# Kernel optimization log

Hardware: AMD Instinct MI355X
Metric: run time of the kernel (lower is better)

The kernel has to match this reference:

```python
import jax, jax.numpy as jnp
import numpy as np

B, S, D, H, K = 16, 2048, 1024, 16, 31  # batch, seq, d_model, n_heads, kernel_size


def setup_inputs() -> dict:
    key = jax.random.key(0)
    ks = jax.random.split(key, 6)
    sc = 1.0 / np.sqrt(D)
    return {
        "query_sequences": jax.random.normal(ks[0], (B, S, D), jnp.float32),
        "key_sequences": jax.random.normal(ks[1], (B, S, D), jnp.float32),
        "value_sequences": jax.random.normal(ks[2], (B, S, D), jnp.float32),
        "key_value_sequence_lengths": jax.random.randint(ks[3], (B,), 1, S + 1, jnp.int32),
        "W_q": jax.random.normal(ks[4], (D, H * K), jnp.float32) * sc,  # cast_queries.weight^T
        "b_q": jnp.zeros((H * K,), jnp.float32),                        # cast_queries.bias
        "conv_bias": jnp.zeros((H,), jnp.float32),
    }


def reference(query_sequences, key_sequences, value_sequences,
              key_value_sequence_lengths, W_q, b_q, conv_bias):
    b, s, d = query_sequences.shape
    h = conv_bias.shape[0]
    k = W_q.shape[1] // h
    r = d // h
    # Generate per-position, per-head depthwise filters from the queries.
    weights = (query_sequences @ W_q + b_q).reshape(b, s, h, k)  # (B,S,H,K)
    # Split key channels into heads and reduce within each head -> (B,S,H)
    ksum = key_sequences.reshape(b, s, h, r).sum(axis=-1)
    pad_l = (k - 1) // 2
    pad_r = k - 1 - pad_l
    kpad = jnp.pad(ksum, ((0, 0), (pad_l, pad_r), (0, 0)))  # (B, S+K-1, H)
    # Cross-correlation with per-position filters:
    # out[b,t,h] = sum_j weights[b,t,h,j] * kpad[b, t+j, h]
    out = jnp.zeros((b, s, h), dtype=weights.dtype)
    for j in range(k):  # fixed small kernel loop
        out = out + weights[..., j] * kpad[:, j:j + s, :]
    out = out + conv_bias  # per-head bias
    return out.transpose(0, 2, 1)  # (B, n_heads, S)
```

## Files before the change

### kernel.cpp

```cpp
#include <hip/hip_runtime.h>
#include <hip/hip_bf16.h>

#define BB 16
#define SS 2048
#define DD 1024
#define HH 16
#define KK 31
#define HK 496

typedef float f32x4 __attribute__((ext_vector_type(4)));
typedef __bf16 bf16x8 __attribute__((ext_vector_type(8)));

__device__ __forceinline__ unsigned short f2bf(float x) {
  unsigned u = __float_as_uint(x);
  unsigned r = u + 0x7FFFu + ((u >> 16) & 1u);
  return (unsigned short)(r >> 16);
}

__global__ void prep_kernel(const float* __restrict__ Wq,
                            unsigned short* __restrict__ Bimg) {
  int idx = blockIdx.x * 256 + threadIdx.x;
  int e = idx & 7;
  int qq = (idx >> 3) & 15;
  int g = (idx >> 7) & 3;
  int n = (idx >> 9) & 3;
  int w = (idx >> 11) & 7;
  int ks = idx >> 14;
  int k = ks * 32 + g * 8 + e;
  int c = w * 64 + n * 16 + qq;
  int h = c >> 5, j = c & 31;
  float v = (j < KK) ? Wq[k * HK + h * KK + j] : 0.f;
  Bimg[idx] = f2bf(v);
}

__global__ void ksum_kernel(const float* __restrict__ key,
                            float* __restrict__ ksum) {
  const int row = blockIdx.x;
  const int tid = threadIdx.x;
  const float4 v = reinterpret_cast<const float4*>(key + (size_t)row * DD)[tid];
  float p = v.x + v.y + v.z + v.w;
  p += __shfl_xor(p, 1);
  p += __shfl_xor(p, 2);
  p += __shfl_xor(p, 4);
  p += __shfl_xor(p, 8);
  if ((tid & 15) == 0) ksum[(size_t)row * HH + (tid >> 4)] = p;
}

__global__ __launch_bounds__(512, 4) void mca_kernel(
    const float* __restrict__ q, const float* __restrict__ bq,
    const float* __restrict__ convb, const float* __restrict__ ksum,
    const unsigned short* __restrict__ Bimg, float* __restrict__ out) {
  __shared__ char smem[8192];
  const int tid = threadIdx.x;
  const int w = tid >> 6, lane = tid & 63;
  const int g = lane >> 4, qq = lane & 15;
  const int bid = blockIdx.x;
  const int bb = bid >> 5;
  const int t0 = (bid & 31) << 6;

  char* const bA0 = smem;
  char* const bA1 = smem + 4096;

  const float* qblk = q + ((size_t)(bb * SS + t0)) * DD;
  const unsigned short* bbase = Bimg + w * 2048 + lane * 8;

  f32x4 acc[4][4];
#pragma unroll
  for (int m = 0; m < 4; ++m)
#pragma unroll
    for (int n = 0; n < 4; ++n) acc[m][n] = (f32x4){0.f, 0.f, 0.f, 0.f};

  const int arow = tid >> 3;
  const int apart = tid & 7;
  const int ag = apart >> 1, ah = apart & 1;

  auto issueA = [&](int ks, float4& rA) {
    rA = *reinterpret_cast<const float4*>(qblk + (size_t)arow * DD + ks * 32 + apart * 4);
  };
  auto writeA = [&](char* dst, const float4& rA) {
    unsigned u0 = (unsigned)f2bf(rA.x) | ((unsigned)f2bf(rA.y) << 16);
    unsigned u1 = (unsigned)f2bf(rA.z) | ((unsigned)f2bf(rA.w) << 16);
    *reinterpret_cast<uint2*>(dst + ag * 1024 + arow * 16 + ah * 8) = make_uint2(u0, u1);
  };
  auto loadB = [&](int ks, bf16x8* pB) {
    const unsigned short* p = bbase + (size_t)ks * 16384;
#pragma unroll
    for (int n = 0; n < 4; ++n)
      pB[n] = *reinterpret_cast<const bf16x8*>(p + n * 512);
  };
  auto computeT = [&](const char* bufA, const bf16x8* pB) {
    bf16x8 af[4];
#pragma unroll
    for (int m = 0; m < 4; ++m)
      af[m] = *reinterpret_cast<const bf16x8*>(bufA + g * 1024 + (m * 16 + qq) * 16);
#pragma unroll
    for (int m = 0; m < 4; ++m)
#pragma unroll
      for (int n = 0; n < 4; ++n)
        acc[m][n] = __builtin_amdgcn_mfma_f32_16x16x32_bf16(af[m], pB[n], acc[m][n], 0, 0, 0);
  };
  auto barrier = [&]() {
    asm volatile("s_waitcnt lgkmcnt(0)" ::: "memory");
    __builtin_amdgcn_s_barrier();
  };

  float4 rA0, rA1;
  bf16x8 pB_a[4], pB_b[4];

  issueA(0, rA0);
  loadB(0, pB_a);
  writeA(bA0, rA0);
  barrier();

  for (int ks2 = 0; ks2 < 15; ++ks2) {
    const int ks = ks2 * 2;
    issueA(ks + 1, rA1);
    loadB(ks + 1, pB_b);
    computeT(bA0, pB_a);
    writeA(bA1, rA1);
    barrier();
    issueA(ks + 2, rA0);
    loadB(ks + 2, pB_a);
    computeT(bA1, pB_b);
    writeA(bA0, rA0);
    barrier();
  }
  issueA(31, rA1);
  loadB(31, pB_b);
  computeT(bA0, pB_a);
  writeA(bA1, rA1);
  barrier();
  computeT(bA1, pB_b);

  float bqv[4];
#pragma unroll
  for (int n = 0; n < 4; ++n) {
    int c = w * 64 + n * 16 + qq;
    int h = c >> 5, j = c & 31;
    bqv[n] = (j < KK) ? bq[h * KK + j] : 0.f;
  }
  float cb[2] = {convb[w * 2], convb[w * 2 + 1]};

  __syncthreads();
  float* kl = reinterpret_cast<float*>(smem);
  for (int i = tid; i < 96 * 16; i += 512) {
    int trow = i >> 4, h = i & 15;
    int t = t0 + trow - 15;
    kl[trow * 17 + h] = (t >= 0 && t < SS) ? ksum[((size_t)bb * SS + t) * HH + h] : 0.f;
  }
  __syncthreads();

#pragma unroll
  for (int m = 0; m < 4; ++m) {
    float part[4][2];
#pragma unroll
    for (int r = 0; r < 4; ++r) {
      part[r][0] = 0.f;
      part[r][1] = 0.f;
    }
#pragma unroll
    for (int n = 0; n < 4; ++n) {
      const int hp = n >> 1;
      const int j = (n & 1) * 16 + qq;
      const int h = w * 2 + hp;
#pragma unroll
      for (int r = 0; r < 4; ++r) {
        const int tl = m * 16 + g * 4 + r;
        part[r][hp] += (acc[m][n][r] + bqv[n]) * kl[(tl + j) * 17 + h];
      }
    }
#pragma unroll
    for (int r = 0; r < 4; ++r)
#pragma unroll
      for (int hp = 0; hp < 2; ++hp) {
        float v = part[r][hp];
        v += __shfl_xor(v, 1);
        v += __shfl_xor(v, 2);
        v += __shfl_xor(v, 4);
        v += __shfl_xor(v, 8);
        part[r][hp] = v;
      }
    if (qq < 4) {
      const int r = qq;
      const int t = t0 + m * 16 + g * 4 + r;
#pragma unroll
      for (int hp = 0; hp < 2; ++hp)
        out[((size_t)bb * HH + w * 2 + hp) * SS + t] = part[r][hp] + cb[hp];
    }
  }
}

extern "C" void kernel_launch(void* const* d_in, const int* in_sizes, int n_in,
                              void* d_out, int out_size, void* d_ws, size_t ws_size,
                              hipStream_t stream) {
  const float* q   = (const float*)d_in[0];
  const float* key = (const float*)d_in[1];
  const float* Wq  = (const float*)d_in[4];
  const float* bq  = (const float*)d_in[5];
  const float* cvb = (const float*)d_in[6];
  float* out = (float*)d_out;

  float* ksum = (float*)d_ws;
  unsigned short* Bimg = (unsigned short*)((char*)d_ws + 2097152);

  prep_kernel<<<2048, 256, 0, stream>>>(Wq, Bimg);
  ksum_kernel<<<BB * SS, 256, 0, stream>>>(key, ksum);
  mca_kernel<<<BB * (SS / 64), 512, 0, stream>>>(q, bq, cvb, ksum, Bimg, out);
}
```

Baseline: 79.06 us.

## Stage full bf16 query tile in LDS up front and drop per-step barriers

Each block now loads its whole 64x1024 query tile, converts it to bf16 and writes it into 128KB of dynamic LDS with an XOR swizzle before the MFMA loop. This replaces the double-buffered per-k-step A staging and its barriers. The inner loop then only prefetches B fragments from global memory. The large LDS footprint cuts occupancy, with launch bounds lowered to 2, and all load latency is exposed up front instead of overlapped with compute.

```diff
diff --git a/kernel.cpp b/kernel.cpp
--- a/kernel.cpp
+++ b/kernel.cpp
@@ -46,20 +46,17 @@
   if ((tid & 15) == 0) ksum[(size_t)row * HH + (tid >> 4)] = p;
 }
 
-__global__ __launch_bounds__(512, 4) void mca_kernel(
+__global__ __launch_bounds__(512, 2) void mca_kernel(
     const float* __restrict__ q, const float* __restrict__ bq,
     const float* __restrict__ convb, const float* __restrict__ ksum,
     const unsigned short* __restrict__ Bimg, float* __restrict__ out) {
-  __shared__ char smem[8192];
+  extern __shared__ char smem[];
   const int tid = threadIdx.x;
   const int w = tid >> 6, lane = tid & 63;
   const int g = lane >> 4, qq = lane & 15;
   const int bid = blockIdx.x;
   const int bb = bid >> 5;
   const int t0 = (bid & 31) << 6;
-
-  char* const bA0 = smem;
-  char* const bA1 = smem + 4096;
 
   const float* qblk = q + ((size_t)(bb * SS + t0)) * DD;
   const unsigned short* bbase = Bimg + w * 2048 + lane * 8;
@@ -70,67 +67,50 @@
 #pragma unroll
     for (int n = 0; n < 4; ++n) acc[m][n] = (f32x4){0.f, 0.f, 0.f, 0.f};
 
-  const int arow = tid >> 3;
-  const int apart = tid & 7;
-  const int ag = apart >> 1, ah = apart & 1;
+#pragma unroll 8
+  for (int it = 0; it < 32; ++it) {
+    const int gidx = it * 512 + tid;
+    const int row = gidx >> 8;
+    const int c16 = gidx & 255;
+    const float4 v = reinterpret_cast<const float4*>(qblk)[gidx];
+    const int ks = c16 >> 3, gg = (c16 >> 1) & 3, half = c16 & 1;
+    const unsigned u0 = (unsigned)f2bf(v.x) | ((unsigned)f2bf(v.y) << 16);
+    const unsigned u1 = (unsigned)f2bf(v.z) | ((unsigned)f2bf(v.w) << 16);
+    const int byte = (ks * 4096 + gg * 1024 + row * 16 + half * 8) ^ ((ks & 7) << 4);
+    *reinterpret_cast<uint2*>(smem + byte) = make_uint2(u0, u1);
+  }
+  __syncthreads();
 
-  auto issueA = [&](int ks, float4& rA) {
-    rA = *reinterpret_cast<const float4*>(qblk + (size_t)arow * DD + ks * 32 + apart * 4);
-  };
-  auto writeA = [&](char* dst, const float4& rA) {
-    unsigned u0 = (unsigned)f2bf(rA.x) | ((unsigned)f2bf(rA.y) << 16);
-    unsigned u1 = (unsigned)f2bf(rA.z) | ((unsigned)f2bf(rA.w) << 16);
-    *reinterpret_cast<uint2*>(dst + ag * 1024 + arow * 16 + ah * 8) = make_uint2(u0, u1);
-  };
   auto loadB = [&](int ks, bf16x8* pB) {
     const unsigned short* p = bbase + (size_t)ks * 16384;
 #pragma unroll
     for (int n = 0; n < 4; ++n)
       pB[n] = *reinterpret_cast<const bf16x8*>(p + n * 512);
   };
-  auto computeT = [&](const char* bufA, const bf16x8* pB) {
+  auto compute = [&](int ks, const bf16x8* pB) {
+    const int sw = (ks & 7) << 4;
     bf16x8 af[4];
 #pragma unroll
-    for (int m = 0; m < 4; ++m)
-      af[m] = *reinterpret_cast<const bf16x8*>(bufA + g * 1024 + (m * 16 + qq) * 16);
+    for (int m = 0; m < 4; ++m) {
+      const int byte = (ks * 4096 + g * 1024 + (m * 16 + qq) * 16) ^ sw;
+      af[m] = *reinterpret_cast<const bf16x8*>(smem + byte);
+    }
 #pragma unroll
     for (int m = 0; m < 4; ++m)
 #pragma unroll
       for (int n = 0; n < 4; ++n)
         acc[m][n] = __builtin_amdgcn_mfma_f32_16x16x32_bf16(af[m], pB[n], acc[m][n], 0, 0, 0);
   };
-  auto barrier = [&]() {
-    asm volatile("s_waitcnt lgkmcnt(0)" ::: "memory");
-    __builtin_amdgcn_s_barrier();
-  };
 
-  float4 rA0, rA1;
-  bf16x8 pB_a[4], pB_b[4];
-
-  issueA(0, rA0);
-  loadB(0, pB_a);
-  writeA(bA0, rA0);
-  barrier();
-
-  for (int ks2 = 0; ks2 < 15; ++ks2) {
-    const int ks = ks2 * 2;
-    issueA(ks + 1, rA1);
-    loadB(ks + 1, pB_b);
-    computeT(bA0, pB_a);
-    writeA(bA1, rA1);
-    barrier();
-    issueA(ks + 2, rA0);
-    loadB(ks + 2, pB_a);
-    computeT(bA1, pB_b);
-    writeA(bA0, rA0);
-    barrier();
+  bf16x8 pBa[4], pBb[4];
+  loadB(0, pBa);
+#pragma unroll
+  for (int k2 = 0; k2 < 16; ++k2) {
+    loadB(2 * k2 + 1, pBb);
+    compute(2 * k2, pBa);
+    if (k2 < 15) loadB(2 * k2 + 2, pBa);
+    compute(2 * k2 + 1, pBb);
   }
-  issueA(31, rA1);
-  loadB(31, pB_b);
-  computeT(bA0, pB_a);
-  writeA(bA1, rA1);
-  barrier();
-  computeT(bA1, pB_b);
 
   float bqv[4];
 #pragma unroll
@@ -203,7 +183,10 @@
   float* ksum = (float*)d_ws;
   unsigned short* Bimg = (unsigned short*)((char*)d_ws + 2097152);
 
+  hipFuncSetAttribute((const void*)mca_kernel,
+                      hipFuncAttributeMaxDynamicSharedMemorySize, 131072);
+
   prep_kernel<<<2048, 256, 0, stream>>>(Wq, Bimg);
   ksum_kernel<<<BB * SS, 256, 0, stream>>>(key, ksum);
-  mca_kernel<<<BB * (SS / 64), 512, 0, stream>>>(q, bq, cvb, ksum, Bimg, out);
+  mca_kernel<<<BB * (SS / 64), 512, 131072, stream>>>(q, bq, cvb, ksum, Bimg, out);
 }
```

Measured after the change: 91.30 us. +15.5%, slower.

## Switch projection GEMM to 32x32x16 bf16 MFMA tiles with matching layouts

Applied to the files above, without the earlier changes.

Replaces the 16x16x32 MFMA tiling (4x4 accumulators per wave) with 32x32x16 MFMA (2x2 f32x16 accumulators), reorganising the prepacked W_q image and the shared-memory A layout to fit the new operand format. The epilogue is rewritten so each 32-wide column tile maps exactly to one head's filter taps, reducing across 32 lanes with one more shuffle step. The aim is fewer MFMA issues and fewer A-fragment LDS reads per K step. In exchange the epilogue does more shuffle reductions with many masked single-lane stores, and register pressure changes.

```diff
diff --git a/kernel.cpp b/kernel.cpp
--- a/kernel.cpp
+++ b/kernel.cpp
@@ -8,29 +8,29 @@
 #define KK 31
 #define HK 496
 
-typedef float f32x4 __attribute__((ext_vector_type(4)));
+typedef float f32x16 __attribute__((ext_vector_type(16)));
 typedef __bf16 bf16x8 __attribute__((ext_vector_type(8)));
 
-__device__ __forceinline__ unsigned short f2bf(float x) {
+__device__ __forceinline__ unsigned f2bf(float x) {
   unsigned u = __float_as_uint(x);
   unsigned r = u + 0x7FFFu + ((u >> 16) & 1u);
-  return (unsigned short)(r >> 16);
+  return r >> 16;
 }
 
 __global__ void prep_kernel(const float* __restrict__ Wq,
                             unsigned short* __restrict__ Bimg) {
   int idx = blockIdx.x * 256 + threadIdx.x;
   int e = idx & 7;
-  int qq = (idx >> 3) & 15;
-  int g = (idx >> 7) & 3;
-  int n = (idx >> 9) & 3;
-  int w = (idx >> 11) & 7;
+  int lane = (idx >> 3) & 63;
+  int nt = (idx >> 9) & 1;
+  int w = (idx >> 10) & 7;
+  int slice = (idx >> 13) & 1;
   int ks = idx >> 14;
-  int k = ks * 32 + g * 8 + e;
-  int c = w * 64 + n * 16 + qq;
+  int k = ks * 32 + slice * 16 + (lane >> 5) * 8 + e;
+  int c = w * 64 + nt * 32 + (lane & 31);
   int h = c >> 5, j = c & 31;
   float v = (j < KK) ? Wq[k * HK + h * KK + j] : 0.f;
-  Bimg[idx] = f2bf(v);
+  Bimg[idx] = (unsigned short)f2bf(v);
 }
 
 __global__ void ksum_kernel(const float* __restrict__ key,
@@ -53,7 +53,7 @@
   __shared__ char smem[8192];
   const int tid = threadIdx.x;
   const int w = tid >> 6, lane = tid & 63;
-  const int g = lane >> 4, qq = lane & 15;
+  const int l31 = lane & 31, hi = lane >> 5;
   const int bid = blockIdx.x;
   const int bb = bid >> 5;
   const int t0 = (bid & 31) << 6;
@@ -62,42 +62,52 @@
   char* const bA1 = smem + 4096;
 
   const float* qblk = q + ((size_t)(bb * SS + t0)) * DD;
-  const unsigned short* bbase = Bimg + w * 2048 + lane * 8;
+  const unsigned short* bbase = Bimg + (((size_t)w * 2) << 9) + lane * 8;
 
-  f32x4 acc[4][4];
+  f32x16 acc[2][2];
 #pragma unroll
-  for (int m = 0; m < 4; ++m)
+  for (int mt = 0; mt < 2; ++mt)
 #pragma unroll
-    for (int n = 0; n < 4; ++n) acc[m][n] = (f32x4){0.f, 0.f, 0.f, 0.f};
+    for (int nt = 0; nt < 2; ++nt)
+#pragma unroll
+      for (int r = 0; r < 16; ++r) acc[mt][nt][r] = 0.f;
 
   const int arow = tid >> 3;
-  const int apart = tid & 7;
-  const int ag = apart >> 1, ah = apart & 1;
+  const int ak4 = tid & 7;
+  const int as = ak4 >> 2, ah = (ak4 >> 1) & 1, ae = ak4 & 1;
+  const int abyte = as * 2048 + ah * 1024 + arow * 16 + ae * 8;
 
   auto issueA = [&](int ks, float4& rA) {
-    rA = *reinterpret_cast<const float4*>(qblk + (size_t)arow * DD + ks * 32 + apart * 4);
+    rA = *reinterpret_cast<const float4*>(qblk + (size_t)arow * DD + ks * 32 + ak4 * 4);
   };
   auto writeA = [&](char* dst, const float4& rA) {
-    unsigned u0 = (unsigned)f2bf(rA.x) | ((unsigned)f2bf(rA.y) << 16);
-    unsigned u1 = (unsigned)f2bf(rA.z) | ((unsigned)f2bf(rA.w) << 16);
-    *reinterpret_cast<uint2*>(dst + ag * 1024 + arow * 16 + ah * 8) = make_uint2(u0, u1);
+    unsigned u0 = f2bf(rA.x) | (f2bf(rA.y) << 16);
+    unsigned u1 = f2bf(rA.z) | (f2bf(rA.w) << 16);
+    *reinterpret_cast<uint2*>(dst + abyte) = make_uint2(u0, u1);
   };
-  auto loadB = [&](int ks, bf16x8* pB) {
+  auto loadB = [&](int ks, bf16x8 pB[2][2]) {
     const unsigned short* p = bbase + (size_t)ks * 16384;
 #pragma unroll
-    for (int n = 0; n < 4; ++n)
-      pB[n] = *reinterpret_cast<const bf16x8*>(p + n * 512);
+    for (int s = 0; s < 2; ++s)
+#pragma unroll
+      for (int nt = 0; nt < 2; ++nt)
+        pB[s][nt] = *reinterpret_cast<const bf16x8*>(p + (s * 16 + nt) * 512);
   };
-  auto computeT = [&](const char* bufA, const bf16x8* pB) {
-    bf16x8 af[4];
+  auto computeT = [&](const char* bufA, const bf16x8 pB[2][2]) {
 #pragma unroll
-    for (int m = 0; m < 4; ++m)
-      af[m] = *reinterpret_cast<const bf16x8*>(bufA + g * 1024 + (m * 16 + qq) * 16);
+    for (int s = 0; s < 2; ++s) {
+      bf16x8 a[2];
 #pragma unroll
-    for (int m = 0; m < 4; ++m)
+      for (int mt = 0; mt < 2; ++mt)
+        a[mt] = *reinterpret_cast<const bf16x8*>(
+            bufA + s * 2048 + hi * 1024 + (mt * 32 + l31) * 16);
 #pragma unroll
-      for (int n = 0; n < 4; ++n)
-        acc[m][n] = __builtin_amdgcn_mfma_f32_16x16x32_bf16(af[m], pB[n], acc[m][n], 0, 0, 0);
+      for (int mt = 0; mt < 2; ++mt)
+#pragma unroll
+        for (int nt = 0; nt < 2; ++nt)
+          acc[mt][nt] = __builtin_amdgcn_mfma_f32_32x32x16_bf16(
+              a[mt], pB[s][nt], acc[mt][nt], 0, 0, 0);
+    }
   };
   auto barrier = [&]() {
     asm volatile("s_waitcnt lgkmcnt(0)" ::: "memory");
@@ -105,41 +115,40 @@
   };
 
   float4 rA0, rA1;
-  bf16x8 pB_a[4], pB_b[4];
+  bf16x8 pBa[2][2], pBb[2][2];
 
   issueA(0, rA0);
-  loadB(0, pB_a);
+  loadB(0, pBa);
   writeA(bA0, rA0);
   barrier();
 
   for (int ks2 = 0; ks2 < 15; ++ks2) {
     const int ks = ks2 * 2;
     issueA(ks + 1, rA1);
-    loadB(ks + 1, pB_b);
-    computeT(bA0, pB_a);
+    loadB(ks + 1, pBb);
+    computeT(bA0, pBa);
     writeA(bA1, rA1);
     barrier();
     issueA(ks + 2, rA0);
-    loadB(ks + 2, pB_a);
-    computeT(bA1, pB_b);
+    loadB(ks + 2, pBa);
+    computeT(bA1, pBb);
     writeA(bA0, rA0);
     barrier();
   }
   issueA(31, rA1);
-  loadB(31, pB_b);
-  computeT(bA0, pB_a);
+  loadB(31, pBb);
+  computeT(bA0, pBa);
   writeA(bA1, rA1);
   barrier();
-  computeT(bA1, pB_b);
+  computeT(bA1, pBb);
 
-  float bqv[4];
+  float bqv[2], cb[2];
 #pragma unroll
-  for (int n = 0; n < 4; ++n) {
-    int c = w * 64 + n * 16 + qq;
-    int h = c >> 5, j = c & 31;
-    bqv[n] = (j < KK) ? bq[h * KK + j] : 0.f;
+  for (int nt = 0; nt < 2; ++nt) {
+    const int h = w * 2 + nt;
+    bqv[nt] = (l31 < KK) ? bq[h * KK + l31] : 0.f;
+    cb[nt] = convb[h];
   }
-  float cb[2] = {convb[w * 2], convb[w * 2 + 1]};
 
   __syncthreads();
   float* kl = reinterpret_cast<float*>(smem);
@@ -151,43 +160,23 @@
   __syncthreads();
 
 #pragma unroll
-  for (int m = 0; m < 4; ++m) {
-    float part[4][2];
+  for (int mt = 0; mt < 2; ++mt)
 #pragma unroll
-    for (int r = 0; r < 4; ++r) {
-      part[r][0] = 0.f;
-      part[r][1] = 0.f;
-    }
+    for (int nt = 0; nt < 2; ++nt) {
+      const int h = w * 2 + nt;
 #pragma unroll
-    for (int n = 0; n < 4; ++n) {
-      const int hp = n >> 1;
-      const int j = (n & 1) * 16 + qq;
-      const int h = w * 2 + hp;
-#pragma unroll
-      for (int r = 0; r < 4; ++r) {
-        const int tl = m * 16 + g * 4 + r;
-        part[r][hp] += (acc[m][n][r] + bqv[n]) * kl[(tl + j) * 17 + h];
-      }
-    }
-#pragma unroll
-    for (int r = 0; r < 4; ++r)
-#pragma unroll
-      for (int hp = 0; hp < 2; ++hp) {
-        float v = part[r][hp];
+      for (int r = 0; r < 16; ++r) {
+        const int tl = mt * 32 + (r & 3) + 8 * (r >> 2) + 4 * hi;
+        float v = (acc[mt][nt][r] + bqv[nt]) * kl[(tl + l31) * 17 + h];
         v += __shfl_xor(v, 1);
         v += __shfl_xor(v, 2);
         v += __shfl_xor(v, 4);
         v += __shfl_xor(v, 8);
-        part[r][hp] = v;
+        v += __shfl_xor(v, 16);
+        if (l31 == r)
+          out[((size_t)(bb * HH + h)) * SS + t0 + tl] = v + cb[nt];
       }
-    if (qq < 4) {
-      const int r = qq;
-      const int t = t0 + m * 16 + g * 4 + r;
-#pragma unroll
-      for (int hp = 0; hp < 2; ++hp)
-        out[((size_t)bb * HH + w * 2 + hp) * SS + t] = part[r][hp] + cb[hp];
     }
-  }
 }
 
 extern "C" void kernel_launch(void* const* d_in, const int* in_sizes, int n_in,
@@ -201,7 +190,7 @@
   float* out = (float*)d_out;
 
   float* ksum = (float*)d_ws;
-  unsigned short* Bimg = (unsigned short*)((char*)d_ws + 2097152);
+  unsigned short* Bimg = (unsigned short*)((char*)d_ws + (2 << 20));
 
   prep_kernel<<<2048, 256, 0, stream>>>(Wq, Bimg);
   ksum_kernel<<<BB * SS, 256, 0, stream>>>(key, ksum);
```

Measured after the change: 90.31 us. +14.2%, slower.
